# Performance work log

Measured on AMD Instinct MI355X. Metric: run time of the kernel, lower is better.

The kernel has to match this reference:

```python
import jax, jax.numpy as jnp
import numpy as np

K = 20      # knn fan-in (constructor arg)
EPS = 1e-5  # LayerNorm eps (torch default)

def ln(x, g, b):
    m = jnp.mean(x, axis=-1, keepdims=True)
    v = jnp.mean((x - m) ** 2, axis=-1, keepdims=True)
    return (x - m) / jnp.sqrt(v + EPS) * g + b

def setup_inputs():
    key = jax.random.key(0)
    ks = jax.random.split(key, 12)
    N, Cin, Cout, H = 4096, 128, 128, 512
    def w(k, i, o):
        return (jax.random.normal(k, (i, o), jnp.float32) / np.sqrt(i)).astype(jnp.float32)
    return dict(
        x=jax.random.normal(ks[0], (N, Cin), jnp.float32),
        pos=jax.random.normal(ks[1], (N, 3), jnp.float32),
        batch=jnp.zeros((N,), jnp.int32),
        # PointTransformerConv linears (bias=False in PyG)
        W_lin=w(ks[2], Cin, Cout),
        W_src=w(ks[3], Cin, Cout),
        W_dst=w(ks[4], Cin, Cout),
        # pos_nn: Lin(3,H) LN ELU Lin(H,Cout) LN ELU
        pw1=w(ks[5], 3, H), pb1=jnp.zeros((H,), jnp.float32),
        pg1=jnp.ones((H,), jnp.float32), pbt1=jnp.zeros((H,), jnp.float32),
        pw2=w(ks[6], H, Cout), pb2=jnp.zeros((Cout,), jnp.float32),
        pg2=jnp.ones((Cout,), jnp.float32), pbt2=jnp.zeros((Cout,), jnp.float32),
        # attn_nn: Lin(Cout,H) LN ELU Lin(H,Cout) LN ELU
        aw1=w(ks[7], Cout, H), ab1=jnp.zeros((H,), jnp.float32),
        ag1=jnp.ones((H,), jnp.float32), abt1=jnp.zeros((H,), jnp.float32),
        aw2=w(ks[8], H, Cout), ab2=jnp.zeros((Cout,), jnp.float32),
        ag2=jnp.ones((Cout,), jnp.float32), abt2=jnp.zeros((Cout,), jnp.float32),
    )

def knn_idx(pos):
    # single-graph knn (batch is constant zero); returns [N, K+1] neighbor idx
    # with self-loop appended (PointTransformerConv add_self_loops=True).
    N = pos.shape[0]
    sq = jnp.sum(pos * pos, axis=1)
    d2 = sq[:, None] + sq[None, :] - 2.0 * (pos @ pos.T)      # [N, N]
    d2 = d2.at[jnp.arange(N), jnp.arange(N)].set(jnp.inf)      # loop=False
    _, nbr = jax.lax.top_k(-d2, K)                             # [N, K]
    return jnp.concatenate([nbr, jnp.arange(N)[:, None]], axis=1)

def reference(x, pos, batch, W_lin, W_src, W_dst,
              pw1, pb1, pg1, pbt1, pw2, pb2, pg2, pbt2,
              aw1, ab1, ag1, abt1, aw2, ab2, ag2, abt2):
    idx = knn_idx(pos)                      # [N, K+1] source node per edge
    v = x @ W_lin                           # message values
    a_src = x @ W_src
    a_dst = x @ W_dst
    rel = pos[:, None, :] - pos[idx]        # pos_i - pos_j, [N, K+1, 3]
    h = jax.nn.elu(ln(rel @ pw1 + pb1, pg1, pbt1))
    delta = jax.nn.elu(ln(h @ pw2 + pb2, pg2, pbt2))           # [N, K+1, C]
    alpha = a_dst[:, None, :] - a_src[idx] + delta
    h2 = jax.nn.elu(ln(alpha @ aw1 + ab1, ag1, abt1))
    alpha = jax.nn.elu(ln(h2 @ aw2 + ab2, ag2, abt2))
    alpha = jax.nn.softmax(alpha, axis=1)   # softmax over neighbors of i
    return jnp.sum(alpha * (v[idx] + delta), axis=1)           # [N, C]
```

## Files before the change

### kernel.cpp

```cpp
#include <hip/hip_runtime.h>
#include <math.h>

#define NN    4096
#define CIN   128
#define CO    128
#define HD    512
#define KK    20
#define EE    21
#define EDGES (NN * EE)
#define LNEPS 1e-5f
#define WSZ   65536

typedef unsigned short u16;
typedef unsigned int   u32;
typedef unsigned long long u64;
typedef __attribute__((ext_vector_type(8))) short bf16x8;
typedef __attribute__((ext_vector_type(4))) float f32x4;

#define MFMA16(a,b,c) __builtin_amdgcn_mfma_f32_16x16x32_bf16(a,b,c,0,0,0)

__device__ __forceinline__ u16 f2b(float x) {
    u32 u = __float_as_uint(x);
    u32 r = u + 0x7fffu + ((u >> 16) & 1u);
    return (u16)(r >> 16);
}
__device__ __forceinline__ float b2f(u16 h) {
    return __uint_as_float(((u32)h) << 16);
}

__global__ __launch_bounds__(64) void k_knn(const float* __restrict__ pos,
                                            int* __restrict__ idxg)
{
    int i = blockIdx.x;
    int lane = threadIdx.x;
    float px = pos[3*i], py = pos[3*i+1], pz = pos[3*i+2];
    float bd[KK]; int bi[KK];
#pragma unroll
    for (int s = 0; s < KK; ++s) { bd[s] = INFINITY; bi[s] = 0x7fffffff; }
    for (int j = lane; j < NN; j += 64) {
        float dx = px - pos[3*j], dy = py - pos[3*j+1], dz = pz - pos[3*j+2];
        float d2 = dx*dx + dy*dy + dz*dz;
        if (j != i && d2 < bd[KK-1]) {
            float cd = d2; int ci = j;
#pragma unroll
            for (int s = 0; s < KK; ++s) {
                bool sw = cd < bd[s];
                float td = sw ? bd[s] : cd;  int ti = sw ? bi[s] : ci;
                bd[s] = sw ? cd : bd[s];     bi[s] = sw ? ci : bi[s];
                cd = td; ci = ti;
            }
        }
    }
    for (int r = 0; r < KK; ++r) {
        u64 m = ~0ull;
#pragma unroll
        for (int s = 0; s < KK; ++s) {
            u64 k = ((u64)__float_as_uint(bd[s]) << 32) | (u32)bi[s];
            m = k < m ? k : m;
        }
#pragma unroll
        for (int off = 32; off > 0; off >>= 1) {
            u64 o = __shfl_xor(m, off, 64);
            m = o < m ? o : m;
        }
        if (lane == 0) idxg[i*EE + r] = (int)(u32)m;
#pragma unroll
        for (int s = 0; s < KK; ++s) {
            u64 k = ((u64)__float_as_uint(bd[s]) << 32) | (u32)bi[s];
            if (k == m) bd[s] = INFINITY;
        }
    }
    if (lane == 0) idxg[i*EE + KK] = i;
}

__global__ __launch_bounds__(256) void k_lin3(const float* __restrict__ x,
        const float* __restrict__ Wl, const float* __restrict__ Ws, const float* __restrict__ Wd,
        float* __restrict__ v, float* __restrict__ as_, float* __restrict__ ad)
{
    __shared__ float sx[8][CIN];
    int b = blockIdx.x, t = threadIdx.x;
    int n0 = b * 8;
    for (int q = t; q < 8*CIN; q += 256) sx[q >> 7][q & 127] = x[n0*CIN + q];
    __syncthreads();
    int c = t & 127, g = t >> 7;
    float al[4] = {0,0,0,0}, asr[4] = {0,0,0,0}, adr[4] = {0,0,0,0};
    for (int k = 0; k < CIN; ++k) {
        float wl = Wl[k*CO + c], ws = Ws[k*CO + c], wd = Wd[k*CO + c];
#pragma unroll
        for (int nn2 = 0; nn2 < 4; ++nn2) {
            float xv = sx[g*4 + nn2][k];
            al[nn2]  = fmaf(xv, wl, al[nn2]);
            asr[nn2] = fmaf(xv, ws, asr[nn2]);
            adr[nn2] = fmaf(xv, wd, adr[nn2]);
        }
    }
#pragma unroll
    for (int nn2 = 0; nn2 < 4; ++nn2) {
        int n = n0 + g*4 + nn2;
        v[n*CO + c]   = al[nn2];
        as_[n*CO + c] = asr[nn2];
        ad[n*CO + c]  = adr[nn2];
    }
}

__global__ __launch_bounds__(256) void k_wconv3(
        const float* __restrict__ aw1, const float* __restrict__ aw2,
        const float* __restrict__ pw2,
        u16* __restrict__ awp1, u16* __restrict__ awp2, u16* __restrict__ pwp2)
{
    int gb = blockIdx.x;
    const float* src; u16* dst; int N, kplog, base; bool split;
    if (gb < 256)      { src = aw1; dst = awp1; N = HD; kplog = 2; base = 0;   split = false; }
    else if (gb < 512) { src = aw2; dst = awp2; N = CO; kplog = 4; base = 256; split = true;  }
    else               { src = pw2; dst = pwp2; N = CO; kplog = 4; base = 512; split = true;  }
    int idx = (gb - base)*256 + threadIdx.x;
    int j  = idx & 7;
    int l  = (idx >> 3) & 63;
    int ks = (idx >> 9) & ((1 << kplog) - 1);
    int nt = idx >> (9 + kplog);
    int k = ks*32 + (l >> 4)*8 + j;
    int c = nt*16 + (l & 15);
    float w = src[(size_t)k*N + c];
    u16 hi = f2b(w);
    dst[idx] = hi;
    if (split) dst[idx + WSZ] = f2b(w - b2f(hi));
}

template<int L, int NW>
__device__ __forceinline__ void ln_elu_b16(u16* base, int rows, int stride,
        const float* __restrict__ gam, const float* __restrict__ bet)
{
    constexpr int P = L / 64;
    int t = threadIdx.x, lane = t & 63, w = t >> 6;
    float g[P], b[P];
#pragma unroll
    for (int q = 0; q < P; q += 4) {
        *(float4*)&g[q] = *(const float4*)&gam[lane*P + q];
        *(float4*)&b[q] = *(const float4*)&bet[lane*P + q];
    }
    for (int e = w; e < rows; e += NW) {
        u16* row = base + e*stride + lane*P;
        u16 raw[P];
        *(ushort4*)&raw[0] = *(const ushort4*)&row[0];
        *(ushort4*)&raw[4] = *(const ushort4*)&row[4];
        float vals[P]; float s = 0.f, sq = 0.f;
#pragma unroll
        for (int q = 0; q < P; ++q) {
            float xx = b2f(raw[q]);
            vals[q] = xx; s += xx; sq = fmaf(xx, xx, sq);
        }
#pragma unroll
        for (int off = 32; off > 0; off >>= 1) {
            s  += __shfl_xor(s,  off, 64);
            sq += __shfl_xor(sq, off, 64);
        }
        float mn = s * (1.0f / L);
        float msq = mn * mn;
        float var = fmaf(sq, 1.0f / L, -msq);
        float rstd = rsqrtf(var + LNEPS);
#pragma unroll
        for (int q = 0; q < P; ++q) {
            float z = (vals[q] - mn) * rstd;
            float y = fmaf(z, g[q], b[q]);
            y = y > 0.f ? y : __expf(y) - 1.f;
            raw[q] = f2b(y);
        }
        *(ushort4*)&row[0] = *(const ushort4*)&raw[0];
        *(ushort4*)&row[4] = *(const ushort4*)&raw[4];
    }
}

template<int L, int NW>
__device__ __forceinline__ void ln_elu_f32v(float* base, int rows, int stride,
        const float* __restrict__ gam, const float* __restrict__ bet)
{
    constexpr int P = L / 64;
    int t = threadIdx.x, lane = t & 63, w = t >> 6;
    float g[P], b[P];
    *(float2*)&g[0] = *(const float2*)&gam[lane*P];
    *(float2*)&b[0] = *(const float2*)&bet[lane*P];
    for (int e = w; e < rows; e += NW) {
        float* row = base + e*stride + lane*P;
        float vals[P];
        *(float2*)&vals[0] = *(const float2*)&row[0];
        float s = 0.f, sq = 0.f;
#pragma unroll
        for (int q = 0; q < P; ++q) { s += vals[q]; sq = fmaf(vals[q], vals[q], sq); }
#pragma unroll
        for (int off = 32; off > 0; off >>= 1) {
            s  += __shfl_xor(s,  off, 64);
            sq += __shfl_xor(sq, off, 64);
        }
        float mn = s * (1.0f / L);
        float msq = mn * mn;
        float var = fmaf(sq, 1.0f / L, -msq);
        float rstd = rsqrtf(var + LNEPS);
#pragma unroll
        for (int q = 0; q < P; ++q) {
            float z = (vals[q] - mn) * rstd;
            float y = fmaf(z, g[q], b[q]);
            vals[q] = y > 0.f ? y : __expf(y) - 1.f;
        }
        *(float2*)&row[0] = *(const float2*)&vals[0];
    }
}

#define SA_S 136
#define SH_S 520
#define SF_S 132

__global__ __launch_bounds__(512) void k_posnn(
        const float* __restrict__ pos, const int* __restrict__ idxg,
        const float* __restrict__ pw1, const float* __restrict__ pb1,
        const float* __restrict__ pg1, const float* __restrict__ pbt1,
        const u16* __restrict__ pwp2, const float* __restrict__ pb2,
        const float* __restrict__ pg2, const float* __restrict__ pbt2,
        u16* __restrict__ delta)
{
    __shared__ __align__(16) u16   s_h[32*SH_S];
    __shared__ __align__(16) float s_d[32*SF_S];
    __shared__ float s_rel[32][3];
    int t = threadIdx.x;
    int e0g = blockIdx.x * 32;
    if (t < 32) {
        int e = e0g + t;
        u32 ii = (u32)e / 21u;
        int j = idxg[e];
        s_rel[t][0] = pos[3*ii]   - pos[3*j];
        s_rel[t][1] = pos[3*ii+1] - pos[3*j+1];
        s_rel[t][2] = pos[3*ii+2] - pos[3*j+2];
    }
    __syncthreads();
    {
        int c1 = t;
        float wa0 = pw1[c1], wa1 = pw1[HD + c1], wa2 = pw1[2*HD + c1], ba = pb1[c1];
        for (int r = 0; r < 32; ++r) {
            float hv = fmaf(s_rel[r][2], wa2, fmaf(s_rel[r][1], wa1, fmaf(s_rel[r][0], wa0, ba)));
            s_h[r*SH_S + c1] = f2b(hv);
        }
    }
    __syncthreads();
    ln_elu_b16<HD, 8>(s_h, 32, SH_S, pg1, pbt1);
    __syncthreads();
    {
        int w = t >> 6, l = t & 63, lr = l & 15, lk = l >> 4;
        int m = w & 1, nt0 = (w >> 1) * 2;
        bf16x8 afr[16];
#pragma unroll
        for (int ks = 0; ks < 16; ++ks)
            afr[ks] = *(const bf16x8*)&s_h[(m*16 + lr)*SH_S + ks*32 + lk*8];
#pragma unroll
        for (int n2 = 0; n2 < 2; ++n2) {
            int nt = nt0 + n2;
            const u16* bp  = pwp2 + ((size_t)nt*16*64 + l)*8;
            const u16* bpl = bp + WSZ;
            f32x4 acc = {0.f, 0.f, 0.f, 0.f};
#pragma unroll
            for (int ks = 0; ks < 16; ++ks) {
                bf16x8 bh = *(const bf16x8*)(bp + ks*512);
                acc = MFMA16(afr[ks], bh, acc);
                bf16x8 bl = *(const bf16x8*)(bpl + ks*512);
                acc = MFMA16(afr[ks], bl, acc);
            }
            float bias = pb2[nt*16 + lr];
#pragma unroll
            for (int r = 0; r < 4; ++r)
                s_d[(m*16 + lk*4 + r)*SF_S + nt*16 + lr] = acc[r] + bias;
        }
    }
    __syncthreads();
    ln_elu_f32v<CO, 8>(s_d, 32, SF_S, pg2, pbt2);
    __syncthreads();
    {
        int el = t >> 4, c0 = (t & 15) << 3;
        const float* sp = &s_d[el*SF_S + c0];
        float4 v0 = *(const float4*)(sp);
        float4 v1 = *(const float4*)(sp + 4);
        bf16x8 o;
        o[0] = (short)f2b(v0.x); o[1] = (short)f2b(v0.y);
        o[2] = (short)f2b(v0.z); o[3] = (short)f2b(v0.w);
        o[4] = (short)f2b(v1.x); o[5] = (short)f2b(v1.y);
        o[6] = (short)f2b(v1.z); o[7] = (short)f2b(v1.w);
        *(bf16x8*)&delta[(size_t)(e0g + el)*CO + c0] = o;
    }
}

__global__ __launch_bounds__(512) void k_amlp(
        const int* __restrict__ idxg,
        const float* __restrict__ as_, const float* __restrict__ ad,
        const u16* __restrict__ delta,
        const u16* __restrict__ awp1, const float* __restrict__ ab1,
        const float* __restrict__ ag1, const float* __restrict__ abt1,
        const u16* __restrict__ awp2, const float* __restrict__ ab2,
        const float* __restrict__ ag2, const float* __restrict__ abt2,
        u16* __restrict__ alphaF)
{
    __shared__ __align__(16) u16   s_h[32*SH_S];
    __shared__ __align__(16) float s_u[32*SF_S];
    u16*   s_a  = (u16*)s_u;
    float* s_af = s_u;
    int t = threadIdx.x;
    int e0g = blockIdx.x * 32;
    {
        int el = t >> 4, c0 = (t & 15) << 3;
        int e = e0g + el;
        int i = (int)((u32)e / 21u);
        int j = idxg[e];
        const float* adp = ad  + i*CIN + c0;
        const float* asp = as_ + j*CIN + c0;
        const u16*  dp   = delta + (size_t)e*CO + c0;
        float4 a0 = *(const float4*)(adp);
        float4 a1 = *(const float4*)(adp + 4);
        float4 s0 = *(const float4*)(asp);
        float4 s1 = *(const float4*)(asp + 4);
        bf16x8 d8 = *(const bf16x8*)(dp);
        bf16x8 o;
        o[0] = (short)f2b(a0.x - s0.x + b2f((u16)d8[0]));
        o[1] = (short)f2b(a0.y - s0.y + b2f((u16)d8[1]));
        o[2] = (short)f2b(a0.z - s0.z + b2f((u16)d8[2]));
        o[3] = (short)f2b(a0.w - s0.w + b2f((u16)d8[3]));
        o[4] = (short)f2b(a1.x - s1.x + b2f((u16)d8[4]));
        o[5] = (short)f2b(a1.y - s1.y + b2f((u16)d8[5]));
        o[6] = (short)f2b(a1.z - s1.z + b2f((u16)d8[6]));
        o[7] = (short)f2b(a1.w - s1.w + b2f((u16)d8[7]));
        *(bf16x8*)&s_a[el*SA_S + c0] = o;
    }
    __syncthreads();
    int w = t >> 6, l = t & 63, lr = l & 15, lk = l >> 4;
    {
        int m = w & 1, nt0 = (w >> 1) * 8;
        bf16x8 afr[4];
#pragma unroll
        for (int ks = 0; ks < 4; ++ks)
            afr[ks] = *(const bf16x8*)&s_a[(m*16 + lr)*SA_S + ks*32 + lk*8];
#pragma unroll
        for (int n2 = 0; n2 < 8; ++n2) {
            int nt = nt0 + n2;
            const u16* bp = awp1 + ((size_t)nt*4*64 + l)*8;
            f32x4 acc = {0.f, 0.f, 0.f, 0.f};
#pragma unroll
            for (int ks = 0; ks < 4; ++ks) {
                bf16x8 bfr = *(const bf16x8*)(bp + ks*512);
                acc = MFMA16(afr[ks], bfr, acc);
            }
            float bias = ab1[nt*16 + lr];
#pragma unroll
            for (int r = 0; r < 4; ++r)
                s_h[(m*16 + lk*4 + r)*SH_S + nt*16 + lr] = f2b(acc[r] + bias);
        }
    }
    __syncthreads();
    ln_elu_b16<HD, 8>(s_h, 32, SH_S, ag1, abt1);
    __syncthreads();
    {
        int m = w & 1, nt0 = (w >> 1) * 2;
        bf16x8 afr[16];
#pragma unroll
        for (int ks = 0; ks < 16; ++ks)
            afr[ks] = *(const bf16x8*)&s_h[(m*16 + lr)*SH_S + ks*32 + lk*8];
#pragma unroll
        for (int n2 = 0; n2 < 2; ++n2) {
            int nt = nt0 + n2;
            const u16* bp  = awp2 + ((size_t)nt*16*64 + l)*8;
            const u16* bpl = bp + WSZ;
            f32x4 acc = {0.f, 0.f, 0.f, 0.f};
#pragma unroll
            for (int ks = 0; ks < 16; ++ks) {
                bf16x8 bh = *(const bf16x8*)(bp + ks*512);
                acc = MFMA16(afr[ks], bh, acc);
                bf16x8 bl = *(const bf16x8*)(bpl + ks*512);
                acc = MFMA16(afr[ks], bl, acc);
            }
            float bias = ab2[nt*16 + lr];
#pragma unroll
            for (int r = 0; r < 4; ++r)
                s_af[(m*16 + lk*4 + r)*SF_S + nt*16 + lr] = acc[r] + bias;
        }
    }
    __syncthreads();
    ln_elu_f32v<CO, 8>(s_af, 32, SF_S, ag2, abt2);
    __syncthreads();
    {
        int el = t >> 4, c0 = (t & 15) << 3;
        const float* sp = &s_af[el*SF_S + c0];
        float4 v0 = *(const float4*)(sp);
        float4 v1 = *(const float4*)(sp + 4);
        bf16x8 o;
        o[0] = (short)f2b(v0.x); o[1] = (short)f2b(v0.y);
        o[2] = (short)f2b(v0.z); o[3] = (short)f2b(v0.w);
        o[4] = (short)f2b(v1.x); o[5] = (short)f2b(v1.y);
        o[6] = (short)f2b(v1.z); o[7] = (short)f2b(v1.w);
        *(bf16x8*)&alphaF[(size_t)(e0g + el)*CO + c0] = o;
    }
}

__global__ __launch_bounds__(256) void k_agg(
        const int* __restrict__ idxg,
        const float* __restrict__ v, const u16* __restrict__ delta,
        const u16* __restrict__ alphaF, float* __restrict__ out)
{
    __shared__ int s_idx[2][EE];
    int b = blockIdx.x, t = threadIdx.x;
    int n0 = b * 2;
    if (t < 2*EE) s_idx[t/EE][t%EE] = idxg[n0*EE + t];
    __syncthreads();
    int c = t & 127, g = t >> 7;
    int i = n0 + g;
    size_t base = (size_t)i*EE*CO + c;
    float af[EE]; float mx = -INFINITY;
#pragma unroll
    for (int e = 0; e < EE; ++e) { af[e] = b2f(alphaF[base + e*CO]); mx = fmaxf(mx, af[e]); }
    float ssum = 0.f;
#pragma unroll
    for (int e = 0; e < EE; ++e) { af[e] = __expf(af[e] - mx); ssum += af[e]; }
    float accv = 0.f;
#pragma unroll
    for (int e = 0; e < EE; ++e) {
        int j = s_idx[g][e];
        float msg = v[j*CO + c] + b2f(delta[base + e*CO]);
        accv = fmaf(af[e], msg, accv);
    }
    out[i*CO + c] = accv / ssum;
}

extern "C" void kernel_launch(void* const* d_in, const int* in_sizes, int n_in,
                              void* d_out, int out_size, void* d_ws, size_t ws_size,
                              hipStream_t stream)
{
    const float* x    = (const float*)d_in[0];
    const float* pos  = (const float*)d_in[1];
    const float* Wl   = (const float*)d_in[3];
    const float* Wsrc = (const float*)d_in[4];
    const float* Wdst = (const float*)d_in[5];
    const float* pw1  = (const float*)d_in[6];
    const float* pb1  = (const float*)d_in[7];
    const float* pg1  = (const float*)d_in[8];
    const float* pbt1 = (const float*)d_in[9];
    const float* pw2  = (const float*)d_in[10];
    const float* pb2  = (const float*)d_in[11];
    const float* pg2  = (const float*)d_in[12];
    const float* pbt2 = (const float*)d_in[13];
    const float* aw1  = (const float*)d_in[14];
    const float* ab1  = (const float*)d_in[15];
    const float* ag1  = (const float*)d_in[16];
    const float* abt1 = (const float*)d_in[17];
    const float* aw2  = (const float*)d_in[18];
    const float* ab2  = (const float*)d_in[19];
    const float* ag2  = (const float*)d_in[20];
    const float* abt2 = (const float*)d_in[21];
    float* out = (float*)d_out;

    char* ws = (char*)d_ws;
    int*   idxg   = (int*)ws;
    u16*   awp1   = (u16*)(ws + 0x54000);
    u16*   awp2   = (u16*)(ws + 0x74000);
    u16*   pwp2   = (u16*)(ws + 0xB4000);
    float* v      = (float*)(ws + 0x100000);
    float* asrc   = (float*)(ws + 0x300000);
    float* adst   = (float*)(ws + 0x500000);
    u16*   delta  = (u16*)(ws + 0x700000);
    u16*   alphaF = (u16*)(ws + 0x700000 + 0x1500000);

    k_knn   <<<NN,       64,  0, stream>>>(pos, idxg);
    k_wconv3<<<768,      256, 0, stream>>>(aw1, aw2, pw2, awp1, awp2, pwp2);
    k_lin3  <<<NN/8,     256, 0, stream>>>(x, Wl, Wsrc, Wdst, v, asrc, adst);
    k_posnn <<<EDGES/32, 512, 0, stream>>>(pos, idxg, pw1, pb1, pg1, pbt1,
                                           pwp2, pb2, pg2, pbt2, delta);
    k_amlp  <<<EDGES/32, 512, 0, stream>>>(idxg, asrc, adst, delta,
                                           awp1, ab1, ag1, abt1,
                                           awp2, ab2, ag2, abt2, alphaF);
    k_agg   <<<NN/2,     256, 0, stream>>>(idxg, v, delta, alphaF, out);
}
```

Measured before the change: 295.0 us.

## Pack four queries per kNN block, split MFMA accumulators, vectorize aggregation

```diff
diff --git a/kernel.cpp b/kernel.cpp
--- a/kernel.cpp
+++ b/kernel.cpp
@@ -28,11 +28,11 @@
     return __uint_as_float(((u32)h) << 16);
 }
 
-__global__ __launch_bounds__(64) void k_knn(const float* __restrict__ pos,
-                                            int* __restrict__ idxg)
-{
-    int i = blockIdx.x;
-    int lane = threadIdx.x;
+__global__ __launch_bounds__(256) void k_knn(const float* __restrict__ pos,
+                                             int* __restrict__ idxg)
+{
+    int i = blockIdx.x * 4 + (threadIdx.x >> 6);
+    int lane = threadIdx.x & 63;
     float px = pos[3*i], py = pos[3*i+1], pz = pos[3*i+2];
     float bd[KK]; int bi[KK];
 #pragma unroll
@@ -254,18 +254,19 @@
             int nt = nt0 + n2;
             const u16* bp  = pwp2 + ((size_t)nt*16*64 + l)*8;
             const u16* bpl = bp + WSZ;
-            f32x4 acc = {0.f, 0.f, 0.f, 0.f};
+            f32x4 acch = {0.f, 0.f, 0.f, 0.f};
+            f32x4 accl = {0.f, 0.f, 0.f, 0.f};
 #pragma unroll
             for (int ks = 0; ks < 16; ++ks) {
                 bf16x8 bh = *(const bf16x8*)(bp + ks*512);
-                acc = MFMA16(afr[ks], bh, acc);
+                acch = MFMA16(afr[ks], bh, acch);
                 bf16x8 bl = *(const bf16x8*)(bpl + ks*512);
-                acc = MFMA16(afr[ks], bl, acc);
+                accl = MFMA16(afr[ks], bl, accl);
             }
             float bias = pb2[nt*16 + lr];
 #pragma unroll
             for (int r = 0; r < 4; ++r)
-                s_d[(m*16 + lk*4 + r)*SF_S + nt*16 + lr] = acc[r] + bias;
+                s_d[(m*16 + lk*4 + r)*SF_S + nt*16 + lr] = (acch[r] + accl[r]) + bias;
         }
     }
     __syncthreads();
@@ -363,18 +364,19 @@
             int nt = nt0 + n2;
             const u16* bp  = awp2 + ((size_t)nt*16*64 + l)*8;
             const u16* bpl = bp + WSZ;
-            f32x4 acc = {0.f, 0.f, 0.f, 0.f};
+            f32x4 acch = {0.f, 0.f, 0.f, 0.f};
+            f32x4 accl = {0.f, 0.f, 0.f, 0.f};
 #pragma unroll
             for (int ks = 0; ks < 16; ++ks) {
                 bf16x8 bh = *(const bf16x8*)(bp + ks*512);
-                acc = MFMA16(afr[ks], bh, acc);
+                acch = MFMA16(afr[ks], bh, acch);
                 bf16x8 bl = *(const bf16x8*)(bpl + ks*512);
-                acc = MFMA16(afr[ks], bl, acc);
+                accl = MFMA16(afr[ks], bl, accl);
             }
             float bias = ab2[nt*16 + lr];
 #pragma unroll
             for (int r = 0; r < 4; ++r)
-                s_af[(m*16 + lk*4 + r)*SF_S + nt*16 + lr] = acc[r] + bias;
+                s_af[(m*16 + lk*4 + r)*SF_S + nt*16 + lr] = (acch[r] + accl[r]) + bias;
         }
     }
     __syncthreads();
@@ -399,28 +401,39 @@
         const float* __restrict__ v, const u16* __restrict__ delta,
         const u16* __restrict__ alphaF, float* __restrict__ out)
 {
-    __shared__ int s_idx[2][EE];
+    __shared__ int s_idx[4][EE];
     int b = blockIdx.x, t = threadIdx.x;
-    int n0 = b * 2;
-    if (t < 2*EE) s_idx[t/EE][t%EE] = idxg[n0*EE + t];
-    __syncthreads();
-    int c = t & 127, g = t >> 7;
+    int n0 = b * 4;
+    if (t < 4*EE) s_idx[t/EE][t%EE] = idxg[n0*EE + t];
+    __syncthreads();
+    int g = t >> 6, c0 = (t & 63) * 2;
     int i = n0 + g;
-    size_t base = (size_t)i*EE*CO + c;
-    float af[EE]; float mx = -INFINITY;
-#pragma unroll
-    for (int e = 0; e < EE; ++e) { af[e] = b2f(alphaF[base + e*CO]); mx = fmaxf(mx, af[e]); }
-    float ssum = 0.f;
-#pragma unroll
-    for (int e = 0; e < EE; ++e) { af[e] = __expf(af[e] - mx); ssum += af[e]; }
-    float accv = 0.f;
+    size_t base = (size_t)i*EE*CO + c0;
+    float afx[EE], afy[EE];
+    float mx0 = -INFINITY, mx1 = -INFINITY;
+#pragma unroll
+    for (int e = 0; e < EE; ++e) {
+        ushort2 u = *(const ushort2*)&alphaF[base + e*CO];
+        afx[e] = b2f(u.x); afy[e] = b2f(u.y);
+        mx0 = fmaxf(mx0, afx[e]); mx1 = fmaxf(mx1, afy[e]);
+    }
+    float ss0 = 0.f, ss1 = 0.f;
+#pragma unroll
+    for (int e = 0; e < EE; ++e) {
+        afx[e] = __expf(afx[e] - mx0); ss0 += afx[e];
+        afy[e] = __expf(afy[e] - mx1); ss1 += afy[e];
+    }
+    float ac0 = 0.f, ac1 = 0.f;
 #pragma unroll
     for (int e = 0; e < EE; ++e) {
         int j = s_idx[g][e];
-        float msg = v[j*CO + c] + b2f(delta[base + e*CO]);
-        accv = fmaf(af[e], msg, accv);
-    }
-    out[i*CO + c] = accv / ssum;
+        float2 vv = *(const float2*)&v[j*CO + c0];
+        ushort2 dd = *(const ushort2*)&delta[base + e*CO];
+        ac0 = fmaf(afx[e], vv.x + b2f(dd.x), ac0);
+        ac1 = fmaf(afy[e], vv.y + b2f(dd.y), ac1);
+    }
+    float2 o; o.x = ac0 / ss0; o.y = ac1 / ss1;
+    *(float2*)&out[i*CO + c0] = o;
 }
 
 extern "C" void kernel_launch(void* const* d_in, const int* in_sizes, int n_in,
@@ -461,7 +474,7 @@
     u16*   delta  = (u16*)(ws + 0x700000);
     u16*   alphaF = (u16*)(ws + 0x700000 + 0x1500000);
 
-    k_knn   <<<NN,       64,  0, stream>>>(pos, idxg);
+    k_knn   <<<NN/4,     256, 0, stream>>>(pos, idxg);
     k_wconv3<<<768,      256, 0, stream>>>(aw1, aw2, pw2, awp1, awp2, pwp2);
     k_lin3  <<<NN/8,     256, 0, stream>>>(x, Wl, Wsrc, Wdst, v, asrc, adst);
     k_posnn <<<EDGES/32, 512, 0, stream>>>(pos, idxg, pw1, pb1, pg1, pbt1,
@@ -469,5 +482,5 @@
     k_amlp  <<<EDGES/32, 512, 0, stream>>>(idxg, asrc, adst, delta,
                                            awp1, ab1, ag1, abt1,
                                            awp2, ab2, ag2, abt2, alphaF);
-    k_agg   <<<NN/2,     256, 0, stream>>>(idxg, v, delta, alphaF, out);
-}
+    k_agg   <<<NN/4,     256, 0, stream>>>(idxg, v, delta, alphaF, out);
+}
```

Result: faster. 279.2 us (-5.4%).
